# Performance work log

Measured on AMD Instinct MI355X. Metric: run time of the kernel, lower is better.

The kernel has to match this reference:

```python
import jax, jax.numpy as jnp
import numpy as np

OUT_F, IN_F = 11008, 4096  # LLaMA-7B up-projection


def setup_inputs() -> dict:
    key = jax.random.key(0)
    k1, k2, k3, k4 = jax.random.split(key, 4)
    x = jax.random.normal(k1, (2, 512, IN_F), dtype=jnp.float32)
    # decoded int8 weights, stored as int32 per spec but valued in [-127, 127]
    weight_int8 = jax.random.randint(k2, (OUT_F, IN_F), -127, 128, dtype=jnp.int32)
    scale = jax.random.uniform(k3, (1,), dtype=jnp.float32) * 0.02 + 1e-3
    bias = jax.random.normal(k4, (OUT_F,), dtype=jnp.float32)
    return {"x": x, "weight_int8": weight_int8, "scale": scale, "bias": bias}


def reference(x, weight_int8, scale, bias):
    # dequantize: int8 * per-tensor scale  (done fresh every forward in original)
    weight = weight_int8.astype(jnp.float32) * scale[0]  # [out, in]
    # F.linear: x @ W^T + b
    out = jnp.einsum('bsi,oi->bso', x, weight) + bias
    return out
```

## Files before the change

kernel.cpp:

```cpp
#include <hip/hip_runtime.h>
#include <hip/hip_bf16.h>


#define M_TOT 1024
#define N_TOT 11008
#define K_TOT 4096
#define BM 256
#define BN 256
#define BKI 128
#define NTI (K_TOT / BKI)
#define ABYTES (BM * BKI)
#define BUFB   ((BM + BN) * BKI)

typedef __attribute__((ext_vector_type(8))) short short8;
typedef __attribute__((ext_vector_type(4))) float f32x4;
typedef __attribute__((ext_vector_type(4))) int   i32x4;

__device__ __forceinline__ unsigned short f2bf(float f) {
    __hip_bfloat16 h = __float2bfloat16(f);
    return __builtin_bit_cast(unsigned short, h);
}

__device__ __forceinline__ void gload16(const void* g, void* l) {
    __builtin_amdgcn_global_load_lds(
        (const __attribute__((address_space(1))) unsigned int*)g,
        (__attribute__((address_space(3))) unsigned int*)l,
        16, 0, 0);
}

#define NPRE 3072

__global__ __launch_bounds__(256)
void prepass_kernel(const int* __restrict__ W, const float* __restrict__ X,
                    int* __restrict__ Wq, int* __restrict__ Xq,
                    float* __restrict__ sx, int wn16) {
    const int t = threadIdx.x;
    if (blockIdx.x < M_TOT) {
        const int r = blockIdx.x;
        const float* xr = X + (size_t)r * K_TOT + t * 16;
        f32x4 v[4];
        float amax = 0.0f;
#pragma unroll
        for (int j = 0; j < 4; ++j) {
            v[j] = *(const f32x4*)(xr + j * 4);
#pragma unroll
            for (int e = 0; e < 4; ++e) amax = fmaxf(amax, fabsf(v[j][e]));
        }
#pragma unroll
        for (int k = 1; k < 64; k <<= 1) amax = fmaxf(amax, __shfl_xor(amax, k));
        __shared__ float sm[4];
        if ((t & 63) == 0) sm[t >> 6] = amax;
        __syncthreads();
        amax = fmaxf(fmaxf(sm[0], sm[1]), fmaxf(sm[2], sm[3]));
        const float inv = (amax > 0.0f) ? (127.0f / amax) : 0.0f;
        if (t == 0) sx[r] = (amax > 0.0f) ? (amax / 127.0f) : 0.0f;
        i32x4 o;
#pragma unroll
        for (int j = 0; j < 4; ++j) {
            int q[4];
#pragma unroll
            for (int e = 0; e < 4; ++e) {
                int qi = (int)rintf(v[j][e] * inv);
                qi = qi > 127 ? 127 : (qi < -127 ? -127 : qi);
                q[e] = qi;
            }
            o[j] = (q[0] & 0xff) | ((q[1] & 0xff) << 8) | ((q[2] & 0xff) << 16) | (q[3] << 24);
        }
        *(i32x4*)(Xq + (size_t)r * (K_TOT / 4) + t * 4) = o;
    } else {
        int idx = (blockIdx.x - M_TOT) * blockDim.x + t;
        int stride = (NPRE - M_TOT) * blockDim.x;
        for (int i = idx; i < wn16; i += stride) {
            const int4* p = (const int4*)W + (size_t)i * 4;
            i32x4 o;
#pragma unroll
            for (int j = 0; j < 4; ++j) {
                int4 v = p[j];
                o[j] = (v.x & 0xff) | ((v.y & 0xff) << 8) | ((v.z & 0xff) << 16) | (v.w << 24);
            }
            *(i32x4*)(Wq + (size_t)i * 4) = o;
        }
    }
}

__global__ __launch_bounds__(512, 2)
void gemm_i8_kernel(const char* __restrict__ Xq,
                    const char* __restrict__ Wq,
                    const float* __restrict__ sx,
                    const float* __restrict__ scale,
                    const float* __restrict__ bias,
                    float* __restrict__ out) {
    __shared__ __align__(16) unsigned char lds[2 * BUFB];

    const int tid  = threadIdx.x;
    const int lane = tid & 63;
    const int wid  = tid >> 6;
    const int wr   = wid >> 2;
    const int wc   = wid & 3;
    const int lr   = lane & 15;
    const int kb   = lane >> 4;

    const int brow = blockIdx.y * BM;
    const int bcol = blockIdx.x * BN;

    const int s_row  = wid * 32 + (lane >> 3);
    const int s_colb = (((lane & 7) ^ (lane >> 3)) * 16);

    const char* asrc0 = Xq + (size_t)(brow + s_row) * K_TOT + s_colb;
    const char* bsrc0 = Wq + (size_t)(bcol + s_row) * K_TOT + s_colb;
    const int lds_row0 = wid * 32;

    auto stageA = [&](int t, unsigned char* buf) {
        const size_t k0 = (size_t)t * BKI;
#pragma unroll
        for (int i = 0; i < 4; ++i)
            gload16(asrc0 + k0 + (size_t)i * 8 * K_TOT, buf + (lds_row0 + i * 8) * BKI);
    };
    auto stageB = [&](int t, unsigned char* buf) {
        const size_t k0 = (size_t)t * BKI;
#pragma unroll
        for (int i = 0; i < 4; ++i)
            gload16(bsrc0 + k0 + (size_t)i * 8 * K_TOT, buf + ABYTES + (lds_row0 + i * 8) * BKI);
    };

    i32x4 acc[8][4];
#pragma unroll
    for (int m = 0; m < 8; ++m)
#pragma unroll
        for (int n = 0; n < 4; ++n)
#pragma unroll
            for (int i = 0; i < 4; ++i) acc[m][n][i] = 0;

    auto do_tile = [&](const unsigned char* cur, unsigned char* nxt, int tn) {
        stageA(tn, nxt);
        asm volatile("s_waitcnt vmcnt(4)" ::: "memory");
        __builtin_amdgcn_s_barrier();
        __builtin_amdgcn_sched_barrier(0);

        i32x4 a0[4], a1[4], a2[4], a3[4], b0[4], b1[4];
        const int c0 = (kb * 16);
        const int c1 = (64 + kb * 16);

#pragma unroll
        for (int n = 0; n < 4; ++n) {
            int row = wc * 64 + n * 16 + lr;
            b0[n] = *(const i32x4*)(cur + ABYTES + row * BKI + (c0 ^ ((row & 7) << 4)));
        }
#pragma unroll
        for (int m = 0; m < 4; ++m) {
            int row = wr * 128 + m * 16 + lr;
            a0[m] = *(const i32x4*)(cur + row * BKI + (c0 ^ ((row & 7) << 4)));
        }
#pragma unroll
        for (int m = 0; m < 4; ++m) {
            int row = wr * 128 + 64 + m * 16 + lr;
            a1[m] = *(const i32x4*)(cur + row * BKI + (c0 ^ ((row & 7) << 4)));
        }

        __builtin_amdgcn_s_setprio(1);
#pragma unroll
        for (int m = 0; m < 4; ++m)
#pragma unroll
            for (int n = 0; n < 4; ++n)
                acc[m][n] = __builtin_amdgcn_mfma_i32_16x16x64_i8(a0[m], b0[n], acc[m][n], 0, 0, 0);
        __builtin_amdgcn_s_setprio(0);

#pragma unroll
        for (int n = 0; n < 4; ++n) {
            int row = wc * 64 + n * 16 + lr;
            b1[n] = *(const i32x4*)(cur + ABYTES + row * BKI + (c1 ^ ((row & 7) << 4)));
        }
#pragma unroll
        for (int m = 0; m < 4; ++m) {
            int row = wr * 128 + m * 16 + lr;
            a2[m] = *(const i32x4*)(cur + row * BKI + (c1 ^ ((row & 7) << 4)));
        }

        __builtin_amdgcn_s_setprio(1);
#pragma unroll
        for (int m = 0; m < 4; ++m)
#pragma unroll
            for (int n = 0; n < 4; ++n)
                acc[4 + m][n] = __builtin_amdgcn_mfma_i32_16x16x64_i8(a1[m], b0[n], acc[4 + m][n], 0, 0, 0);
        __builtin_amdgcn_s_setprio(0);

#pragma unroll
        for (int m = 0; m < 4; ++m) {
            int row = wr * 128 + 64 + m * 16 + lr;
            a3[m] = *(const i32x4*)(cur + row * BKI + (c1 ^ ((row & 7) << 4)));
        }
        stageB(tn, nxt);

        __builtin_amdgcn_s_setprio(1);
#pragma unroll
        for (int m = 0; m < 4; ++m)
#pragma unroll
            for (int n = 0; n < 4; ++n)
                acc[m][n] = __builtin_amdgcn_mfma_i32_16x16x64_i8(a2[m], b1[n], acc[m][n], 0, 0, 0);
        __builtin_amdgcn_s_setprio(0);

        __builtin_amdgcn_s_setprio(1);
#pragma unroll
        for (int m = 0; m < 4; ++m)
#pragma unroll
            for (int n = 0; n < 4; ++n)
                acc[4 + m][n] = __builtin_amdgcn_mfma_i32_16x16x64_i8(a3[m], b1[n], acc[4 + m][n], 0, 0, 0);
        __builtin_amdgcn_s_setprio(0);

        asm volatile("s_waitcnt lgkmcnt(0)" ::: "memory");
        __builtin_amdgcn_s_barrier();
    };

    unsigned char* buf0 = lds;
    unsigned char* buf1 = lds + BUFB;

    stageA(0, buf0);
    stageB(0, buf0);

    for (int t = 0; t < NTI; t += 2) {
        do_tile(buf0, buf1, t + 1);
        do_tile(buf1, buf0, (t + 2 < NTI) ? t + 2 : 0);
    }

    const float sw = scale[0];
    const int orow0 = brow + wr * 128;
    const int ocol0 = bcol + wc * 64;
    float bv[4];
#pragma unroll
    for (int n = 0; n < 4; ++n) bv[n] = bias[ocol0 + n * 16 + lr];
#pragma unroll
    for (int m = 0; m < 8; ++m) {
        f32x4 sx4 = *(const f32x4*)(sx + orow0 + m * 16 + kb * 4);
#pragma unroll
        for (int i = 0; i < 4; ++i) {
            int r = orow0 + m * 16 + kb * 4 + i;
            size_t base = (size_t)r * N_TOT + ocol0;
            float fs = sx4[i] * sw;
#pragma unroll
            for (int n = 0; n < 4; ++n)
                out[base + n * 16 + lr] = (float)acc[m][n][i] * fs + bv[n];
        }
    }
}

__device__ __forceinline__ unsigned long long pack4(float a, float b, float c, float d) {
    return (unsigned long long)f2bf(a)
         | ((unsigned long long)f2bf(b) << 16)
         | ((unsigned long long)f2bf(c) << 32)
         | ((unsigned long long)f2bf(d) << 48);
}

#define FBM 128
#define FBN 128
#define FBK 64
#define FNT (K_TOT / FBK)

__global__ __launch_bounds__(256, 2)
void otf_linear_fused(const float* __restrict__ X, const int* __restrict__ W,
                      const float* __restrict__ scale, const float* __restrict__ bias,
                      float* __restrict__ out) {
    __shared__ __align__(16) unsigned char AsB[FBM * FBK * 2];
    __shared__ __align__(16) unsigned char BsB[FBN * FBK * 2];

    const int tid = threadIdx.x, lane = tid & 63, wid = tid >> 6;
    const int wr = wid >> 1, wc = wid & 1, lr = lane & 15, kb = lane >> 4;
    const int brow = blockIdx.y * FBM, bcol = blockIdx.x * FBN;
    const int srow = tid >> 4, sc4 = tid & 15;

    f32x4 areg[8];
    int4 breg[8];
    auto load_tiles = [&](int t) {
        const int k0 = t * FBK;
#pragma unroll
        for (int p = 0; p < 8; ++p) {
            int row = p * 16 + srow;
            areg[p] = *(const f32x4*)(&X[(size_t)(brow + row) * K_TOT + k0 + sc4 * 4]);
            breg[p] = *(const int4*)(&W[(size_t)(bcol + row) * K_TOT + k0 + sc4 * 4]);
        }
    };
    auto store_tiles = [&]() {
#pragma unroll
        for (int p = 0; p < 8; ++p) {
            int row = p * 16 + srow;
            int boff = (sc4 * 8) ^ ((row & 7) << 4);
            *(unsigned long long*)(&AsB[row * 128 + boff]) =
                pack4(areg[p][0], areg[p][1], areg[p][2], areg[p][3]);
            *(unsigned long long*)(&BsB[row * 128 + boff]) =
                pack4((float)breg[p].x, (float)breg[p].y, (float)breg[p].z, (float)breg[p].w);
        }
    };

    f32x4 acc[4][4];
#pragma unroll
    for (int m = 0; m < 4; ++m)
#pragma unroll
        for (int n = 0; n < 4; ++n)
#pragma unroll
            for (int i = 0; i < 4; ++i) acc[m][n][i] = 0.0f;

    load_tiles(0);
    for (int t = 0; t < FNT; ++t) {
        store_tiles();
        __syncthreads();
        if (t + 1 < FNT) load_tiles(t + 1);
#pragma unroll
        for (int kk = 0; kk < 2; ++kk) {
            short8 af[4], bfr[4];
#pragma unroll
            for (int m = 0; m < 4; ++m) {
                int row = wr * 64 + m * 16 + lr;
                int col = (kk * 64 + kb * 16) ^ ((row & 7) << 4);
                af[m] = *(const short8*)(&AsB[row * 128 + col]);
            }
#pragma unroll
            for (int n = 0; n < 4; ++n) {
                int row = wc * 64 + n * 16 + lr;
                int col = (kk * 64 + kb * 16) ^ ((row & 7) << 4);
                bfr[n] = *(const short8*)(&BsB[row * 128 + col]);
            }
#pragma unroll
            for (int m = 0; m < 4; ++m)
#pragma unroll
                for (int n = 0; n < 4; ++n)
                    acc[m][n] = __builtin_amdgcn_mfma_f32_16x16x32_bf16(af[m], bfr[n], acc[m][n], 0, 0, 0);
        }
        __syncthreads();
    }

    const float sc = scale[0];
    const int orow0 = brow + wr * 64, ocol0 = bcol + wc * 64;
    float bv[4];
#pragma unroll
    for (int n = 0; n < 4; ++n) bv[n] = bias[ocol0 + n * 16 + lr];
#pragma unroll
    for (int m = 0; m < 4; ++m)
#pragma unroll
        for (int i = 0; i < 4; ++i) {
            int r = orow0 + m * 16 + kb * 4 + i;
            size_t base = (size_t)r * N_TOT + ocol0;
#pragma unroll
            for (int n = 0; n < 4; ++n)
                out[base + n * 16 + lr] = acc[m][n][i] * sc + bv[n];
        }
}

extern "C" void kernel_launch(void* const* d_in, const int* in_sizes, int n_in,
                              void* d_out, int out_size, void* d_ws, size_t ws_size,
                              hipStream_t stream) {
    const float* x     = (const float*)d_in[0];
    const int*   w     = (const int*)d_in[1];
    const float* scale = (const float*)d_in[2];
    const float* bias  = (const float*)d_in[3];
    float* out = (float*)d_out;

    const size_t W_ELEMS = (size_t)N_TOT * K_TOT;
    const size_t X_ELEMS = (size_t)M_TOT * K_TOT;
    const size_t need = W_ELEMS + X_ELEMS + M_TOT * sizeof(float);

    if (ws_size >= need) {
        char*  Wq = (char*)d_ws;
        char*  Xq = (char*)d_ws + W_ELEMS;
        float* sx = (float*)((char*)d_ws + W_ELEMS + X_ELEMS);
        prepass_kernel<<<NPRE, 256, 0, stream>>>(w, x, (int*)Wq, (int*)Xq, sx,
                                                 (int)(W_ELEMS / 16));
        gemm_i8_kernel<<<dim3(N_TOT / BN, M_TOT / BM), 512, 0, stream>>>(
            Xq, Wq, sx, scale, bias, out);
    } else {
        otf_linear_fused<<<dim3(N_TOT / FBN, M_TOT / FBM), 256, 0, stream>>>(x, w, scale, bias, out);
    }
}
```

Baseline: 94.75 us.

## Restructure int8 GEMM pipeline into 4-slot K=64 ring buffer with deeper prefetch

Replaces the double-buffered K=128 tiles with a four-slot ring of K=64 half-tiles, issuing A and B loads together three stages ahead. The swizzle pattern and LDS read offsets are redone for 64-byte rows. The goal is to hide global-to-LDS latency better by keeping more loads in flight. The cost is twice as many barriers per K, and the LDS footprint stays at 128KB, which may limit occupancy.

New measurement: 99.97 us. 5.5% more time.

```diff
diff --git a/kernel.cpp b/kernel.cpp
--- a/kernel.cpp
+++ b/kernel.cpp
@@ -7,10 +7,9 @@
 #define K_TOT 4096
 #define BM 256
 #define BN 256
-#define BKI 128
-#define NTI (K_TOT / BKI)
-#define ABYTES (BM * BKI)
-#define BUFB   ((BM + BN) * BKI)
+#define NH (K_TOT / 64)
+#define SLOT_A_SZ 16384
+#define SLOT_B_  32768
 
 typedef __attribute__((ext_vector_type(8))) short short8;
 typedef __attribute__((ext_vector_type(4))) float f32x4;
@@ -90,7 +89,7 @@
                     const float* __restrict__ scale,
                     const float* __restrict__ bias,
                     float* __restrict__ out) {
-    __shared__ __align__(16) unsigned char lds[2 * BUFB];
+    __shared__ __align__(16) unsigned char lds[4 * SLOT_B_];
 
     const int tid  = threadIdx.x;
     const int lane = tid & 63;
@@ -103,25 +102,23 @@
     const int brow = blockIdx.y * BM;
     const int bcol = blockIdx.x * BN;
 
-    const int s_row  = wid * 32 + (lane >> 3);
-    const int s_colb = (((lane & 7) ^ (lane >> 3)) * 16);
+    const int s_row  = wid * 32 + (lane >> 2);
+    const int s_colb = (((lane & 3) ^ ((lane >> 3) & 3)) * 16);
 
     const char* asrc0 = Xq + (size_t)(brow + s_row) * K_TOT + s_colb;
     const char* bsrc0 = Wq + (size_t)(bcol + s_row) * K_TOT + s_colb;
     const int lds_row0 = wid * 32;
 
-    auto stageA = [&](int t, unsigned char* buf) {
-        const size_t k0 = (size_t)t * BKI;
-#pragma unroll
-        for (int i = 0; i < 4; ++i)
-            gload16(asrc0 + k0 + (size_t)i * 8 * K_TOT, buf + (lds_row0 + i * 8) * BKI);
+    auto stage = [&](int h, unsigned char* slot) {
+        const size_t k0 = (size_t)h * 64;
+#pragma unroll
+        for (int i = 0; i < 2; ++i) {
+            gload16(asrc0 + k0 + (size_t)i * 16 * K_TOT, slot + (lds_row0 + i * 16) * 64);
+            gload16(bsrc0 + k0 + (size_t)i * 16 * K_TOT, slot + SLOT_A_SZ + (lds_row0 + i * 16) * 64);
+        }
     };
-    auto stageB = [&](int t, unsigned char* buf) {
-        const size_t k0 = (size_t)t * BKI;
-#pragma unroll
-        for (int i = 0; i < 4; ++i)
-            gload16(bsrc0 + k0 + (size_t)i * 8 * K_TOT, buf + ABYTES + (lds_row0 + i * 8) * BKI);
-    };
+
+    const int rdoff = ((kb ^ ((lr >> 1) & 3)) * 16);
 
     i32x4 acc[8][4];
 #pragma unroll
@@ -131,31 +128,22 @@
 #pragma unroll
             for (int i = 0; i < 4; ++i) acc[m][n][i] = 0;
 
-    auto do_tile = [&](const unsigned char* cur, unsigned char* nxt, int tn) {
-        stageA(tn, nxt);
-        asm volatile("s_waitcnt vmcnt(4)" ::: "memory");
+    auto do_half = [&](const unsigned char* cur, unsigned char* stg, int hn) {
+        stage(hn, stg);
+        asm volatile("s_waitcnt vmcnt(12)" ::: "memory");
         __builtin_amdgcn_s_barrier();
         __builtin_amdgcn_sched_barrier(0);
 
-        i32x4 a0[4], a1[4], a2[4], a3[4], b0[4], b1[4];
-        const int c0 = (kb * 16);
-        const int c1 = (64 + kb * 16);
-
-#pragma unroll
-        for (int n = 0; n < 4; ++n) {
-            int row = wc * 64 + n * 16 + lr;
-            b0[n] = *(const i32x4*)(cur + ABYTES + row * BKI + (c0 ^ ((row & 7) << 4)));
-        }
-#pragma unroll
-        for (int m = 0; m < 4; ++m) {
-            int row = wr * 128 + m * 16 + lr;
-            a0[m] = *(const i32x4*)(cur + row * BKI + (c0 ^ ((row & 7) << 4)));
-        }
-#pragma unroll
-        for (int m = 0; m < 4; ++m) {
-            int row = wr * 128 + 64 + m * 16 + lr;
-            a1[m] = *(const i32x4*)(cur + row * BKI + (c0 ^ ((row & 7) << 4)));
-        }
+        i32x4 a0[4], a1[4], b0[4];
+#pragma unroll
+        for (int n = 0; n < 4; ++n)
+            b0[n] = *(const i32x4*)(cur + SLOT_A_SZ + (wc * 64 + n * 16 + lr) * 64 + rdoff);
+#pragma unroll
+        for (int m = 0; m < 4; ++m)
+            a0[m] = *(const i32x4*)(cur + (wr * 128 + m * 16 + lr) * 64 + rdoff);
+#pragma unroll
+        for (int m = 0; m < 4; ++m)
+            a1[m] = *(const i32x4*)(cur + (wr * 128 + 64 + m * 16 + lr) * 64 + rdoff);
 
         __builtin_amdgcn_s_setprio(1);
 #pragma unroll
@@ -165,17 +153,6 @@
                 acc[m][n] = __builtin_amdgcn_mfma_i32_16x16x64_i8(a0[m], b0[n], acc[m][n], 0, 0, 0);
         __builtin_amdgcn_s_setprio(0);
 
-#pragma unroll
-        for (int n = 0; n < 4; ++n) {
-            int row = wc * 64 + n * 16 + lr;
-            b1[n] = *(const i32x4*)(cur + ABYTES + row * BKI + (c1 ^ ((row & 7) << 4)));
-        }
-#pragma unroll
-        for (int m = 0; m < 4; ++m) {
-            int row = wr * 128 + m * 16 + lr;
-            a2[m] = *(const i32x4*)(cur + row * BKI + (c1 ^ ((row & 7) << 4)));
-        }
-
         __builtin_amdgcn_s_setprio(1);
 #pragma unroll
         for (int m = 0; m < 4; ++m)
@@ -184,42 +161,24 @@
                 acc[4 + m][n] = __builtin_amdgcn_mfma_i32_16x16x64_i8(a1[m], b0[n], acc[4 + m][n], 0, 0, 0);
         __builtin_amdgcn_s_setprio(0);
 
-#pragma unroll
-        for (int m = 0; m < 4; ++m) {
-            int row = wr * 128 + 64 + m * 16 + lr;
-            a3[m] = *(const i32x4*)(cur + row * BKI + (c1 ^ ((row & 7) << 4)));
-        }
-        stageB(tn, nxt);
-
-        __builtin_amdgcn_s_setprio(1);
-#pragma unroll
-        for (int m = 0; m < 4; ++m)
-#pragma unroll
-            for (int n = 0; n < 4; ++n)
-                acc[m][n] = __builtin_amdgcn_mfma_i32_16x16x64_i8(a2[m], b1[n], acc[m][n], 0, 0, 0);
-        __builtin_amdgcn_s_setprio(0);
-
-        __builtin_amdgcn_s_setprio(1);
-#pragma unroll
-        for (int m = 0; m < 4; ++m)
-#pragma unroll
-            for (int n = 0; n < 4; ++n)
-                acc[4 + m][n] = __builtin_amdgcn_mfma_i32_16x16x64_i8(a3[m], b1[n], acc[4 + m][n], 0, 0, 0);
-        __builtin_amdgcn_s_setprio(0);
-
         asm volatile("s_waitcnt lgkmcnt(0)" ::: "memory");
         __builtin_amdgcn_s_barrier();
     };
 
-    unsigned char* buf0 = lds;
-    unsigned char* buf1 = lds + BUFB;
-
-    stageA(0, buf0);
-    stageB(0, buf0);
-
-    for (int t = 0; t < NTI; t += 2) {
-        do_tile(buf0, buf1, t + 1);
-        do_tile(buf1, buf0, (t + 2 < NTI) ? t + 2 : 0);
+    unsigned char* s0 = lds;
+    unsigned char* s1 = lds + SLOT_B_;
+    unsigned char* s2 = lds + 2 * SLOT_B_;
+    unsigned char* s3 = lds + 3 * SLOT_B_;
+
+    stage(0, s0);
+    stage(1, s1);
+    stage(2, s2);
+
+    for (int h = 0; h < NH; h += 4) {
+        do_half(s0, s3, (h + 3) & (NH - 1));
+        do_half(s1, s0, (h + 4) & (NH - 1));
+        do_half(s2, s1, (h + 5) & (NH - 1));
+        do_half(s3, s2, (h + 6) & (NH - 1));
     }
 
     const float sw = scale[0];
```
